# Performance work log

Measured on AMD Instinct MI355X. Metric: run time of the kernel, lower is better.

## Reference

```python
import jax, jax.numpy as jnp
import numpy as np

NUM_HEADS = 4
EPS = 1e-5

def _proj(x, W, b):
    # 1x1x1 Conv3d == channel-wise linear: x [B,C,H,W,D], W [Cout,Cin], b [Cout]
    return jnp.einsum('oc,bchwd->bohwd', W, x) + b[None, :, None, None, None]

def setup_inputs() -> dict:
    key = jax.random.key(0)
    ks = jax.random.split(key, 12)
    B, C, H, W, D = 2, 128, 16, 16, 16
    s = 1.0 / np.sqrt(C)
    inp = {
        'query_features': jax.random.normal(ks[0], (B, C, H, W, D), jnp.float32),
        'key_value_features': jax.random.normal(ks[1], (B, C, H, W, D), jnp.float32),
        'Wq': jax.random.normal(ks[2], (C, C), jnp.float32) * s,
        'bq': jax.random.normal(ks[3], (C,), jnp.float32) * 0.01,
        'Wk': jax.random.normal(ks[4], (C, C), jnp.float32) * s,
        'bk': jax.random.normal(ks[5], (C,), jnp.float32) * 0.01,
        'Wv': jax.random.normal(ks[6], (C, C), jnp.float32) * s,
        'bv': jax.random.normal(ks[7], (C,), jnp.float32) * 0.01,
        'Wo': jax.random.normal(ks[8], (C, C), jnp.float32) * s,
        'bo': jax.random.normal(ks[9], (C,), jnp.float32) * 0.01,
    }
    return inp

def reference(query_features, key_value_features, Wq, bq, Wk, bk, Wv, bv, Wo, bo):
    B, C, H, W, D = query_features.shape
    hd = C // NUM_HEADS  # head_dim
    N = H * W * D
    Q = _proj(query_features, Wq, bq).reshape(B, NUM_HEADS, hd, N)
    K = _proj(key_value_features, Wk, bk).reshape(B, NUM_HEADS, hd, N)
    V = _proj(key_value_features, Wv, bv).reshape(B, NUM_HEADS, hd, N)
    scale = hd ** -0.5
    attn = jnp.einsum('bhdn,bhdm->bhnm', Q, K) * scale  # [B,h,N,N]
    attn = jax.nn.softmax(attn, axis=-1)
    out = jnp.einsum('bhnm,bhdm->bhdn', attn, V).reshape(B, C, H, W, D)
    out = _proj(out, Wo, bo)
    res = query_features + out
    # InstanceNorm3d (affine=False): normalize over spatial dims per (B,C)
    mu = jnp.mean(res, axis=(2, 3, 4), keepdims=True)
    var = jnp.var(res, axis=(2, 3, 4), keepdims=True)
    return (res - mu) * jax.lax.rsqrt(var + EPS)
```

## Files before the change

### kernel.cpp

```cpp
#include <hip/hip_runtime.h>
#include <hip/hip_bf16.h>

typedef unsigned short u16;
typedef unsigned int u32;
typedef __bf16 bf16_t;
typedef bf16_t bf16x8 __attribute__((ext_vector_type(8)));
typedef float f32x4 __attribute__((ext_vector_type(4)));

#define NTOT 4096
#define CCH 128
#define QSCL 0.25503486703f

__device__ __forceinline__ float bf2f(u16 x) {
    return __uint_as_float(((u32)x) << 16);
}
__device__ __forceinline__ u32 pkbf(float a, float b) {
    __hip_bfloat162 h = __float22bfloat162_rn(make_float2(a, b));
    u32 r; __builtin_memcpy(&r, &h, 4); return r;
}
__device__ __forceinline__ u16 f2bf(float a) {
    return (u16)(pkbf(a, a) & 0xffffu);
}

__global__ __launch_bounds__(256, 4) void proj_kernel(
    const float* __restrict__ xq, const float* __restrict__ xkv,
    const float* __restrict__ Wq, const float* __restrict__ bq,
    const float* __restrict__ Wk, const float* __restrict__ bk_,
    const float* __restrict__ Wv, const float* __restrict__ bv_,
    u16* __restrict__ Qt, u16* __restrict__ Kt, u16* __restrict__ Vn)
{
    const int nt = blockIdx.x, p = blockIdx.y, b = blockIdx.z;
    const float* X    = (p == 0) ? xq : xkv;
    const float* Wf   = (p == 0) ? Wq : (p == 1) ? Wk : Wv;
    const float* bias = (p == 0) ? bq : (p == 1) ? bk_ : bv_;
    const float s = (p == 0) ? QSCL : 1.0f;
    const int n0 = nt * 64;
    const int tid = threadIdx.x;

    __shared__ u16 Xt[64 * 128];
    __shared__ u16 Wl[128 * 136];

    #pragma unroll
    for (int k = 0; k < 4; ++k) {
        int n = tid & 63;
        int c = (tid >> 6) + k * 4;
        float f[8];
        #pragma unroll
        for (int j = 0; j < 8; ++j)
            f[j] = X[((size_t)(b * CCH) + 8 * c + j) * NTOT + n0 + n];
        uint4 vv = {pkbf(f[0], f[1]), pkbf(f[2], f[3]), pkbf(f[4], f[5]), pkbf(f[6], f[7])};
        *(uint4*)(Xt + n * 128 + ((c ^ (n & 7)) * 8)) = vv;
    }
    #pragma unroll
    for (int k = 0; k < 8; ++k) {
        int id = tid + k * 256;
        int row = id >> 4;
        int off = (id & 15) * 8;
        const float* wsrc = Wf + row * 128 + off;
        float4 wa = *(const float4*)(wsrc);
        float4 wc = *(const float4*)(wsrc + 4);
        uint4 vv = {pkbf(wa.x * s, wa.y * s), pkbf(wa.z * s, wa.w * s),
                    pkbf(wc.x * s, wc.y * s), pkbf(wc.z * s, wc.w * s)};
        *(uint4*)(Wl + row * 136 + off) = vv;
    }
    __syncthreads();

    const int wave = tid >> 6, lane = tid & 63;
    const int quad = lane >> 4, l16 = lane & 15;
    f32x4 acc[8];
    #pragma unroll
    for (int cf = 0; cf < 8; ++cf) acc[cf] = (f32x4){0.f, 0.f, 0.f, 0.f};

    #pragma unroll
    for (int kk = 0; kk < 4; ++kk) {
        bf16x8 bx = *(const bf16x8*)(Xt + (wave * 16 + l16) * 128 +
                                     (((kk * 4 + quad) ^ (l16 & 7)) * 8));
        #pragma unroll
        for (int cf = 0; cf < 8; ++cf) {
            bf16x8 aw = *(const bf16x8*)(Wl + (cf * 16 + l16) * 136 + kk * 32 + quad * 8);
            acc[cf] = __builtin_amdgcn_mfma_f32_16x16x32_bf16(aw, bx, acc[cf], 0, 0, 0);
        }
    }

    const int n = n0 + wave * 16 + l16;
    #pragma unroll
    for (int cf = 0; cf < 8; ++cf) {
        float4 b4 = *(const float4*)(bias + cf * 16 + quad * 4);
        float v0 = acc[cf][0] + b4.x * s;
        float v1 = acc[cf][1] + b4.y * s;
        float v2 = acc[cf][2] + b4.z * s;
        float v3 = acc[cf][3] + b4.w * s;
        if (p < 2) {
            const int h = cf >> 1;
            const int d0 = (cf & 1) * 16 + quad * 4;
            u16* dst = (p == 0 ? Qt : Kt) + ((size_t)(b * 4 + h) * NTOT + n) * 32 + d0;
            uint2 vv = {pkbf(v0, v1), pkbf(v2, v3)};
            *(uint2*)dst = vv;
        } else {
            int c = cf * 16 + quad * 4;
            u16* dst = Vn + (size_t)(b * CCH + c) * NTOT + n;
            dst[0 * NTOT] = f2bf(v0); dst[1 * NTOT] = f2bf(v1);
            dst[2 * NTOT] = f2bf(v2); dst[3 * NTOT] = f2bf(v3);
        }
    }
}

__global__ __launch_bounds__(256, 2) void flash_attn_kernel(
    const u16* __restrict__ Qt, const u16* __restrict__ Kt,
    const u16* __restrict__ Vn, u16* __restrict__ pO, float* __restrict__ pL)
{
    const int bh = blockIdx.z, kc = blockIdx.y;
    const int wave = threadIdx.x >> 6, lane = threadIdx.x & 63;
    const int q = lane >> 4, l16 = lane & 15;
    const int q0w = blockIdx.x * 256 + wave * 64;

    const u16* Qbh = Qt + (size_t)bh * NTOT * 32;
    const u16* Kbh = Kt + (size_t)bh * NTOT * 32;
    const u16* Vg  = Vn + ((size_t)((bh >> 2) * CCH + (bh & 3) * 32)) * NTOT;

    __shared__ u16 Ksh[8 * 2048];
    __shared__ u16 Vsh[8 * 2048];

    const int kbase = kc * 1024;

    bf16x8 bq[4];
    #pragma unroll
    for (int g = 0; g < 4; ++g)
        bq[g] = *(const bf16x8*)(Qbh + (size_t)(q0w + g * 16 + l16) * 32 + q * 8);

    const size_t kst0 = (size_t)(kbase + wave * 16 + l16) * 32 + q * 8;
    const size_t vst0 = (size_t)((wave & 1) * 16 + l16) * NTOT + kbase +
                        (wave >> 1) * 32 + q * 8;
    const int kds = wave * 512 + lane * 8;
    const int vds = wave * 512 + (q & 1) * 256 + l16 * 8 + (q >> 1) * 4;
    const int frd = lane * 8;

    f32x4 o[4][2];
    #pragma unroll
    for (int g = 0; g < 4; ++g) {
        o[g][0] = (f32x4){0,0,0,0};
        o[g][1] = (f32x4){0,0,0,0};
    }
    const f32x4 zero = {0,0,0,0};
    float lp[4] = {0.f, 0.f, 0.f, 0.f};

    for (int half = 0; half < 2; ++half) {
        if (half)
            __syncthreads();
        {
            const size_t kst = kst0 + (size_t)(half * 512) * 32;
            const size_t vst = vst0 + half * 512;
            #pragma unroll
            for (int m = 0; m < 8; ++m) {
                uint4 kr = *(const uint4*)(Kbh + kst + m * 2048);
                uint4 vr = *(const uint4*)(Vg + vst + m * 64);
                *(uint4*)(&Ksh[m * 2048 + kds]) = kr;
                uint2 va = {vr.x, vr.y};
                uint2 vb = {vr.z, vr.w};
                *(uint2*)(&Vsh[m * 2048 + vds])       = va;
                *(uint2*)(&Vsh[m * 2048 + vds + 128]) = vb;
            }
        }
        __syncthreads();

        bf16x8 ak[4], av[4];
        #pragma unroll
        for (int t = 0; t < 4; ++t) {
            ak[t] = *(const bf16x8*)(&Ksh[t * 512 + frd]);
            av[t] = *(const bf16x8*)(&Vsh[t * 512 + frd]);
        }

        for (int m = 0; m < 8; ++m) {
            bf16x8 nak[4], nav[4];
            if (m < 7) {
                const int nb = (m + 1) * 2048;
                #pragma unroll
                for (int t = 0; t < 4; ++t) {
                    nak[t] = *(const bf16x8*)(&Ksh[nb + t * 512 + frd]);
                    nav[t] = *(const bf16x8*)(&Vsh[nb + t * 512 + frd]);
                }
            }
            f32x4 s[4][4];
            #pragma unroll
            for (int t = 0; t < 4; ++t) {
                #pragma unroll
                for (int g = 0; g < 4; ++g)
                    s[g][t] = __builtin_amdgcn_mfma_f32_16x16x32_bf16(ak[t], bq[g], zero, 0, 0, 0);
            }
            #pragma unroll
            for (int g = 0; g < 4; ++g) {
                float e[4][4];
                #pragma unroll
                for (int t = 0; t < 4; ++t) {
                    e[t][0] = __builtin_amdgcn_exp2f(s[g][t][0]);
                    e[t][1] = __builtin_amdgcn_exp2f(s[g][t][1]);
                    e[t][2] = __builtin_amdgcn_exp2f(s[g][t][2]);
                    e[t][3] = __builtin_amdgcn_exp2f(s[g][t][3]);
                    lp[g] += (e[t][0] + e[t][1]) + (e[t][2] + e[t][3]);
                }
                uint4 u0 = {pkbf(e[0][0], e[0][1]), pkbf(e[0][2], e[0][3]),
                            pkbf(e[1][0], e[1][1]), pkbf(e[1][2], e[1][3])};
                uint4 u1 = {pkbf(e[2][0], e[2][1]), pkbf(e[2][2], e[2][3]),
                            pkbf(e[3][0], e[3][1]), pkbf(e[3][2], e[3][3])};
                bf16x8 pb0, pb1;
                __builtin_memcpy(&pb0, &u0, 16);
                __builtin_memcpy(&pb1, &u1, 16);
                o[g][0] = __builtin_amdgcn_mfma_f32_16x16x32_bf16(av[0], pb0, o[g][0], 0, 0, 0);
                o[g][1] = __builtin_amdgcn_mfma_f32_16x16x32_bf16(av[1], pb0, o[g][1], 0, 0, 0);
                o[g][0] = __builtin_amdgcn_mfma_f32_16x16x32_bf16(av[2], pb1, o[g][0], 0, 0, 0);
                o[g][1] = __builtin_amdgcn_mfma_f32_16x16x32_bf16(av[3], pb1, o[g][1], 0, 0, 0);
            }
            if (m < 7) {
                #pragma unroll
                for (int t = 0; t < 4; ++t) { ak[t] = nak[t]; av[t] = nav[t]; }
            }
        }
    }

    #pragma unroll
    for (int g = 0; g < 4; ++g) {
        lp[g] += __shfl_xor(lp[g], 16);
        lp[g] += __shfl_xor(lp[g], 32);
        const size_t ob = ((size_t)(kc * 8 + bh) * NTOT + q0w + g * 16 + l16) * 32 + q * 4;
        uint2 w0 = {pkbf(o[g][0][0], o[g][0][1]), pkbf(o[g][0][2], o[g][0][3])};
        uint2 w1 = {pkbf(o[g][1][0], o[g][1][1]), pkbf(o[g][1][2], o[g][1][3])};
        *(uint2*)(pO + ob)      = w0;
        *(uint2*)(pO + ob + 16) = w1;
        if (q == 0)
            pL[(size_t)(kc * 8 + bh) * NTOT + q0w + g * 16 + l16] = lp[g];
    }
}

__global__ __launch_bounds__(256, 4) void outproj_kernel(
    const float* __restrict__ xq,
    const u16* __restrict__ pO, const float* __restrict__ pL,
    const float* __restrict__ Wo, const float* __restrict__ bo,
    float* __restrict__ res, float* __restrict__ partS, float* __restrict__ partQ)
{
    const int nt = blockIdx.x, ct = blockIdx.y, b = blockIdx.z;
    const int n0 = nt * 64;
    const int tid = threadIdx.x;

    __shared__ u16 Xt[64 * 128];
    __shared__ u16 Wl[64 * 136];

    #pragma unroll
    for (int k = 0; k < 4; ++k) {
        int cid = tid + k * 256;
        int n = cid >> 4;
        int ch = cid & 15;
        int bh = b * 4 + (ch >> 2);
        int d0 = (ch & 3) * 8;
        float l = 0.f;
        float v[8];
        #pragma unroll
        for (int j = 0; j < 8; ++j) v[j] = 0.f;
        #pragma unroll
        for (int kcc = 0; kcc < 4; ++kcc) {
            const size_t nrow = (size_t)(kcc * 8 + bh) * NTOT + n0 + n;
            l += pL[nrow];
            uint4 u = *(const uint4*)(pO + nrow * 32 + d0);
            const u32 uu[4] = {u.x, u.y, u.z, u.w};
            #pragma unroll
            for (int j = 0; j < 4; ++j) {
                v[2 * j]     += bf2f((u16)(uu[j] & 0xffffu));
                v[2 * j + 1] += bf2f((u16)(uu[j] >> 16));
            }
        }
        const float inv = 1.0f / l;
        uint4 vv = {pkbf(v[0] * inv, v[1] * inv), pkbf(v[2] * inv, v[3] * inv),
                    pkbf(v[4] * inv, v[5] * inv), pkbf(v[6] * inv, v[7] * inv)};
        *(uint4*)(Xt + n * 128 + ((ch ^ (n & 7)) * 8)) = vv;
    }
    #pragma unroll
    for (int k = 0; k < 4; ++k) {
        int id = tid + k * 256;
        int row = id >> 4;
        int off = (id & 15) * 8;
        const float* wsrc = Wo + (size_t)(ct * 64 + row) * 128 + off;
        float4 wa = *(const float4*)(wsrc);
        float4 wc = *(const float4*)(wsrc + 4);
        uint4 vv = {pkbf(wa.x, wa.y), pkbf(wa.z, wa.w),
                    pkbf(wc.x, wc.y), pkbf(wc.z, wc.w)};
        *(uint4*)(Wl + row * 136 + off) = vv;
    }
    __syncthreads();

    const int wave = tid >> 6, lane = tid & 63;
    const int quad = lane >> 4, l16 = lane & 15;
    f32x4 acc[4];
    #pragma unroll
    for (int cf = 0; cf < 4; ++cf) acc[cf] = (f32x4){0.f, 0.f, 0.f, 0.f};

    #pragma unroll
    for (int kk = 0; kk < 4; ++kk) {
        bf16x8 bx = *(const bf16x8*)(Xt + (wave * 16 + l16) * 128 +
                                     (((kk * 4 + quad) ^ (l16 & 7)) * 8));
        #pragma unroll
        for (int cf = 0; cf < 4; ++cf) {
            bf16x8 aw = *(const bf16x8*)(Wl + (cf * 16 + l16) * 136 + kk * 32 + quad * 8);
            acc[cf] = __builtin_amdgcn_mfma_f32_16x16x32_bf16(aw, bx, acc[cf], 0, 0, 0);
        }
    }

    const int n = n0 + wave * 16 + l16;
    const int tile = nt * 4 + wave;
    #pragma unroll
    for (int cf = 0; cf < 4; ++cf) {
        float4 b4 = *(const float4*)(bo + ct * 64 + cf * 16 + quad * 4);
        const float bb[4] = {b4.x, b4.y, b4.z, b4.w};
        float sv[4], qv[4];
        #pragma unroll
        for (int r = 0; r < 4; ++r) {
            int c = ct * 64 + cf * 16 + quad * 4 + r;
            float v = acc[cf][r] + bb[r] + xq[(size_t)(b * CCH + c) * NTOT + n];
            res[(size_t)(b * CCH + c) * NTOT + n] = v;
            sv[r] = v;
            qv[r] = v * v;
        }
        #pragma unroll
        for (int off = 1; off < 16; off <<= 1) {
            #pragma unroll
            for (int r = 0; r < 4; ++r) {
                sv[r] += __shfl_xor(sv[r], off);
                qv[r] += __shfl_xor(qv[r], off);
            }
        }
        if (l16 == 0) {
            #pragma unroll
            for (int r = 0; r < 4; ++r) {
                int c = ct * 64 + cf * 16 + quad * 4 + r;
                partS[(size_t)(b * CCH + c) * 256 + tile] = sv[r];
                partQ[(size_t)(b * CCH + c) * 256 + tile] = qv[r];
            }
        }
    }
}

__global__ __launch_bounds__(256) void norm_kernel(
    const float* __restrict__ res, const float* __restrict__ partS,
    const float* __restrict__ partQ, float* __restrict__ out)
{
    const int c = blockIdx.x, b = blockIdx.y;
    const int tid = threadIdx.x;
    const size_t row = (size_t)(b * CCH + c);
    __shared__ float rs[4], rq[4];
    float s = partS[row * 256 + tid];
    float q = partQ[row * 256 + tid];
    #pragma unroll
    for (int off = 1; off < 64; off <<= 1) {
        s += __shfl_xor(s, off);
        q += __shfl_xor(q, off);
    }
    const int wv = tid >> 6, ln = tid & 63;
    if (ln == 0) { rs[wv] = s; rq[wv] = q; }
    __syncthreads();
    float ts = rs[0] + rs[1] + rs[2] + rs[3];
    float tq = rq[0] + rq[1] + rq[2] + rq[3];
    float mu  = ts * (1.0f / 4096.0f);
    float var = tq * (1.0f / 4096.0f) - mu * mu;
    float inv = rsqrtf(var + 1e-5f);
    const size_t base = row * NTOT;
    #pragma unroll
    for (int j = 0; j < 4; ++j) {
        int n = tid * 4 + j * 1024;
        float4 v = *(const float4*)(res + base + n);
        float4 o;
        o.x = (v.x - mu) * inv; o.y = (v.y - mu) * inv;
        o.z = (v.z - mu) * inv; o.w = (v.w - mu) * inv;
        *(float4*)(out + base + n) = o;
    }
}

extern "C" void kernel_launch(void* const* d_in, const int* in_sizes, int n_in,
                              void* d_out, int out_size, void* d_ws, size_t ws_size,
                              hipStream_t stream)
{
    const float* xq  = (const float*)d_in[0];
    const float* xkv = (const float*)d_in[1];
    const float* Wq  = (const float*)d_in[2];
    const float* bq  = (const float*)d_in[3];
    const float* Wk  = (const float*)d_in[4];
    const float* bk  = (const float*)d_in[5];
    const float* Wv  = (const float*)d_in[6];
    const float* bv  = (const float*)d_in[7];
    const float* Wo  = (const float*)d_in[8];
    const float* bo  = (const float*)d_in[9];
    float* out = (float*)d_out;

    char* ws = (char*)d_ws;
    const size_t MB = (size_t)1 << 20;
    u16* Qt = (u16*)(ws + 0 * MB);
    u16* Kt = (u16*)(ws + 2 * MB);
    u16* Vn = (u16*)(ws + 4 * MB);
    u16* pO = (u16*)(ws + 6 * MB);
    float* pL = (float*)(ws + 14 * MB);
    float* res   = (float*)(ws + 16 * MB);
    float* partS = (float*)(ws + 20 * MB);
    float* partQ = (float*)(ws + 20 * MB + 262144);

    proj_kernel<<<dim3(64, 3, 2), 256, 0, stream>>>(xq, xkv, Wq, bq, Wk, bk, Wv, bv, Qt, Kt, Vn);
    flash_attn_kernel<<<dim3(16, 4, 8), 256, 0, stream>>>(Qt, Kt, Vn, pO, pL);
    outproj_kernel<<<dim3(64, 2, 2), 256, 0, stream>>>(xq, pO, pL, Wo, bo, res, partS, partQ);
    norm_kernel<<<dim3(128, 2), 256, 0, stream>>>(res, partS, partQ, out);
}
```

Baseline: 120.2 us.

## Compute softmax row sums via MFMA and split outproj/norm across more blocks

In the attention kernel, the per-row exp sums are no longer accumulated with VALU adds and cross-lane shuffles. They now come from two extra MFMAs per query group, each multiplying the packed bf16 probabilities by a ones vector. This frees vector ALU time but adds matrix-core work to the inner loop. The output-projection kernel now uses 32-column tiles split over channel halves per wave, doubling its grid. The normalization kernel is split four ways across the spatial dimension, so each block does one vector load and store. Both changes aim to raise parallelism in the small tail kernels, at the cost of redundant partial-stat reads.

```diff
diff --git a/kernel.cpp b/kernel.cpp
--- a/kernel.cpp
+++ b/kernel.cpp
@@ -128,6 +128,13 @@
     for (int g = 0; g < 4; ++g)
         bq[g] = *(const bf16x8*)(Qbh + (size_t)(q0w + g * 16 + l16) * 32 + q * 8);
 
+    bf16x8 aone;
+    {
+        u32 oo = 0x3F803F80u;
+        uint4 uo = {oo, oo, oo, oo};
+        __builtin_memcpy(&aone, &uo, 16);
+    }
+
     const size_t kst0 = (size_t)(kbase + wave * 16 + l16) * 32 + q * 8;
     const size_t vst0 = (size_t)((wave & 1) * 16 + l16) * NTOT + kbase +
                         (wave >> 1) * 32 + q * 8;
@@ -136,13 +143,14 @@
     const int frd = lane * 8;
 
     f32x4 o[4][2];
+    f32x4 ol[4];
     #pragma unroll
     for (int g = 0; g < 4; ++g) {
         o[g][0] = (f32x4){0,0,0,0};
         o[g][1] = (f32x4){0,0,0,0};
+        ol[g]   = (f32x4){0,0,0,0};
     }
     const f32x4 zero = {0,0,0,0};
-    float lp[4] = {0.f, 0.f, 0.f, 0.f};
 
     for (int half = 0; half < 2; ++half) {
         if (half)
@@ -196,7 +204,6 @@
                     e[t][1] = __builtin_amdgcn_exp2f(s[g][t][1]);
                     e[t][2] = __builtin_amdgcn_exp2f(s[g][t][2]);
                     e[t][3] = __builtin_amdgcn_exp2f(s[g][t][3]);
-                    lp[g] += (e[t][0] + e[t][1]) + (e[t][2] + e[t][3]);
                 }
                 uint4 u0 = {pkbf(e[0][0], e[0][1]), pkbf(e[0][2], e[0][3]),
                             pkbf(e[1][0], e[1][1]), pkbf(e[1][2], e[1][3])};
@@ -209,6 +216,8 @@
                 o[g][1] = __builtin_amdgcn_mfma_f32_16x16x32_bf16(av[1], pb0, o[g][1], 0, 0, 0);
                 o[g][0] = __builtin_amdgcn_mfma_f32_16x16x32_bf16(av[2], pb1, o[g][0], 0, 0, 0);
                 o[g][1] = __builtin_amdgcn_mfma_f32_16x16x32_bf16(av[3], pb1, o[g][1], 0, 0, 0);
+                ol[g]   = __builtin_amdgcn_mfma_f32_16x16x32_bf16(aone,  pb0, ol[g],   0, 0, 0);
+                ol[g]   = __builtin_amdgcn_mfma_f32_16x16x32_bf16(aone,  pb1, ol[g],   0, 0, 0);
             }
             if (m < 7) {
                 #pragma unroll
@@ -219,15 +228,13 @@
 
     #pragma unroll
     for (int g = 0; g < 4; ++g) {
-        lp[g] += __shfl_xor(lp[g], 16);
-        lp[g] += __shfl_xor(lp[g], 32);
         const size_t ob = ((size_t)(kc * 8 + bh) * NTOT + q0w + g * 16 + l16) * 32 + q * 4;
         uint2 w0 = {pkbf(o[g][0][0], o[g][0][1]), pkbf(o[g][0][2], o[g][0][3])};
         uint2 w1 = {pkbf(o[g][1][0], o[g][1][1]), pkbf(o[g][1][2], o[g][1][3])};
         *(uint2*)(pO + ob)      = w0;
         *(uint2*)(pO + ob + 16) = w1;
         if (q == 0)
-            pL[(size_t)(kc * 8 + bh) * NTOT + q0w + g * 16 + l16] = lp[g];
+            pL[(size_t)(kc * 8 + bh) * NTOT + q0w + g * 16 + l16] = ol[g][0];
     }
 }
 
@@ -238,14 +245,14 @@
     float* __restrict__ res, float* __restrict__ partS, float* __restrict__ partQ)
 {
     const int nt = blockIdx.x, ct = blockIdx.y, b = blockIdx.z;
-    const int n0 = nt * 64;
+    const int n0 = nt * 32;
     const int tid = threadIdx.x;
 
-    __shared__ u16 Xt[64 * 128];
+    __shared__ u16 Xt[32 * 128];
     __shared__ u16 Wl[64 * 136];
 
     #pragma unroll
-    for (int k = 0; k < 4; ++k) {
+    for (int k = 0; k < 2; ++k) {
         int cid = tid + k * 256;
         int n = cid >> 4;
         int ch = cid & 15;
@@ -288,31 +295,34 @@
 
     const int wave = tid >> 6, lane = tid & 63;
     const int quad = lane >> 4, l16 = lane & 15;
-    f32x4 acc[4];
-    #pragma unroll
-    for (int cf = 0; cf < 4; ++cf) acc[cf] = (f32x4){0.f, 0.f, 0.f, 0.f};
+    const int nh = wave & 1, chh = wave >> 1;
+    f32x4 acc[2];
+    #pragma unroll
+    for (int cf = 0; cf < 2; ++cf) acc[cf] = (f32x4){0.f, 0.f, 0.f, 0.f};
 
     #pragma unroll
     for (int kk = 0; kk < 4; ++kk) {
-        bf16x8 bx = *(const bf16x8*)(Xt + (wave * 16 + l16) * 128 +
+        bf16x8 bx = *(const bf16x8*)(Xt + (nh * 16 + l16) * 128 +
                                      (((kk * 4 + quad) ^ (l16 & 7)) * 8));
         #pragma unroll
-        for (int cf = 0; cf < 4; ++cf) {
-            bf16x8 aw = *(const bf16x8*)(Wl + (cf * 16 + l16) * 136 + kk * 32 + quad * 8);
+        for (int cf = 0; cf < 2; ++cf) {
+            bf16x8 aw = *(const bf16x8*)(Wl + (chh * 32 + cf * 16 + l16) * 136 +
+                                         kk * 32 + quad * 8);
             acc[cf] = __builtin_amdgcn_mfma_f32_16x16x32_bf16(aw, bx, acc[cf], 0, 0, 0);
         }
     }
 
-    const int n = n0 + wave * 16 + l16;
-    const int tile = nt * 4 + wave;
-    #pragma unroll
-    for (int cf = 0; cf < 4; ++cf) {
-        float4 b4 = *(const float4*)(bo + ct * 64 + cf * 16 + quad * 4);
+    const int n = n0 + nh * 16 + l16;
+    const int tile = nt * 2 + nh;
+    #pragma unroll
+    for (int cf = 0; cf < 2; ++cf) {
+        const int cbase = ct * 64 + chh * 32 + cf * 16 + quad * 4;
+        float4 b4 = *(const float4*)(bo + cbase);
         const float bb[4] = {b4.x, b4.y, b4.z, b4.w};
         float sv[4], qv[4];
         #pragma unroll
         for (int r = 0; r < 4; ++r) {
-            int c = ct * 64 + cf * 16 + quad * 4 + r;
+            int c = cbase + r;
             float v = acc[cf][r] + bb[r] + xq[(size_t)(b * CCH + c) * NTOT + n];
             res[(size_t)(b * CCH + c) * NTOT + n] = v;
             sv[r] = v;
@@ -329,7 +339,7 @@
         if (l16 == 0) {
             #pragma unroll
             for (int r = 0; r < 4; ++r) {
-                int c = ct * 64 + cf * 16 + quad * 4 + r;
+                int c = cbase + r;
                 partS[(size_t)(b * CCH + c) * 256 + tile] = sv[r];
                 partQ[(size_t)(b * CCH + c) * 256 + tile] = qv[r];
             }
@@ -341,7 +351,7 @@
     const float* __restrict__ res, const float* __restrict__ partS,
     const float* __restrict__ partQ, float* __restrict__ out)
 {
-    const int c = blockIdx.x, b = blockIdx.y;
+    const int c = blockIdx.x, b = blockIdx.y, zq = blockIdx.z;
     const int tid = threadIdx.x;
     const size_t row = (size_t)(b * CCH + c);
     __shared__ float rs[4], rq[4];
@@ -361,15 +371,12 @@
     float var = tq * (1.0f / 4096.0f) - mu * mu;
     float inv = rsqrtf(var + 1e-5f);
     const size_t base = row * NTOT;
-    #pragma unroll
-    for (int j = 0; j < 4; ++j) {
-        int n = tid * 4 + j * 1024;
-        float4 v = *(const float4*)(res + base + n);
-        float4 o;
-        o.x = (v.x - mu) * inv; o.y = (v.y - mu) * inv;
-        o.z = (v.z - mu) * inv; o.w = (v.w - mu) * inv;
-        *(float4*)(out + base + n) = o;
-    }
+    const int n = tid * 4 + zq * 1024;
+    float4 v = *(const float4*)(res + base + n);
+    float4 o;
+    o.x = (v.x - mu) * inv; o.y = (v.y - mu) * inv;
+    o.z = (v.z - mu) * inv; o.w = (v.w - mu) * inv;
+    *(float4*)(out + base + n) = o;
 }
 
 extern "C" void kernel_launch(void* const* d_in, const int* in_sizes, int n_in,
@@ -401,6 +408,6 @@
 
     proj_kernel<<<dim3(64, 3, 2), 256, 0, stream>>>(xq, xkv, Wq, bq, Wk, bk, Wv, bv, Qt, Kt, Vn);
     flash_attn_kernel<<<dim3(16, 4, 8), 256, 0, stream>>>(Qt, Kt, Vn, pO, pL);
-    outproj_kernel<<<dim3(64, 2, 2), 256, 0, stream>>>(xq, pO, pL, Wo, bo, res, partS, partQ);
-    norm_kernel<<<dim3(128, 2), 256, 0, stream>>>(res, partS, partQ, out);
-}
+    outproj_kernel<<<dim3(128, 2, 2), 256, 0, stream>>>(xq, pO, pL, Wo, bo, res, partS, partQ);
+    norm_kernel<<<dim3(128, 2, 4), 256, 0, stream>>>(res, partS, partQ, out);
+}
```

After: 121.5 us. About the same (+1.1%).
